# Kernel tuning notes

Measured on AMD Instinct MI355X. Metric: run time of the kernel, lower is better.

Reference implementation:

```python
import jax, jax.numpy as jnp
import numpy as np

N_NODES = 50000
N_EDGES = 800000
EPS = 1e-5


def setup_inputs() -> dict:
    key = jax.random.key(0)
    ks = jax.random.split(key, 8)
    x = jax.random.normal(ks[0], (N_NODES, 4), dtype=jnp.float32)
    edge_index = jax.random.randint(ks[1], (2, N_EDGES), 0, N_NODES, dtype=jnp.int64)
    edge_attr = jax.random.normal(ks[2], (N_EDGES, 84), dtype=jnp.float32)
    # nnconv1 (acts as Linear(88,128) over concatenated per-edge features)
    W1 = jax.random.normal(ks[3], (88, 128), dtype=jnp.float32) * (1.0 / np.sqrt(88))
    b1 = jnp.zeros((128,), dtype=jnp.float32)
    # BatchNorm1d(128) affine params
    gamma = jnp.ones((128,), dtype=jnp.float32)
    beta = jnp.zeros((128,), dtype=jnp.float32)
    # node_mlp_2: Linear(132,64) + ReLU
    W2 = jax.random.normal(ks[4], (132, 64), dtype=jnp.float32) * (1.0 / np.sqrt(132))
    b2 = jnp.zeros((64,), dtype=jnp.float32)
    return {"x": x, "edge_index": edge_index, "edge_attr": edge_attr,
            "W1": W1, "b1": b1, "gamma": gamma, "beta": beta, "W2": W2, "b2": b2}


def reference(x, edge_index, edge_attr, W1, b1, gamma, beta, W2, b2):
    row, col = edge_index[0], edge_index[1]
    n_nodes = x.shape[0]
    # gather + concat: [E, 4+84=88]
    h = jnp.concatenate([x[col], edge_attr], axis=1)
    # edge-conditioned linear (NNConv wrapper == Linear(88,128)): [E,128]
    h = h @ W1 + b1
    # BatchNorm1d over edge batch dim (training mode, biased var as torch)
    mean = jnp.mean(h, axis=0)
    var = jnp.mean((h - mean) ** 2, axis=0)
    h = (h - mean) * jax.lax.rsqrt(var + EPS) * gamma + beta
    # scatter_mean over row -> [N,128]
    agg = jax.ops.segment_sum(h, row, num_segments=n_nodes)
    cnt = jax.ops.segment_sum(jnp.ones((h.shape[0],), dtype=h.dtype), row,
                              num_segments=n_nodes)
    agg = agg / jnp.clip(cnt, 1.0)[:, None]
    # concat + MLP: [N, 4+128=132] -> [N,64]
    out = jnp.concatenate([x, agg], axis=1)
    return jax.nn.relu(out @ W2 + b2)
```

## Files before the change

### kernel.cpp

```cpp
#include <hip/hip_runtime.h>
#include <hip/hip_bf16.h>

#define E_EDGES 800000
#define N_NODES_ 50000
#define EPS_ 1e-5f
#define N_SCAN_BLOCKS 49

#define M_GRID   1250
#define M_ITERS  5
#define M_SPLITS 25

#define AGG_EPW  16

typedef float f32x4 __attribute__((ext_vector_type(4)));
typedef short s16x8 __attribute__((ext_vector_type(8)));

#define OFF_M      0
#define OFF_CS     (88 * 88)
#define OFF_CNT    (OFF_CS + 88)
#define OFF_AGG    (OFF_CNT + N_NODES_)
#define ZERO_WORDS (OFF_AGG + N_NODES_ * 88)
#define OFF_CUR    ZERO_WORDS
#define OFF_PART   (OFF_CUR + N_NODES_)
#define OFF_PERM   (OFF_PART + 64)
#define OFF_V      (OFF_PERM + E_EDGES)
#define OFF_S      (OFF_V + 88 * 128)
#define OFF_T      (OFF_S + 128)
#define OFF_MPART  (OFF_T + 128)

__global__ __launch_bounds__(256, 6)
void m_kernel(const float* __restrict__ x, const int* __restrict__ eidx,
              const float* __restrict__ ea, float* __restrict__ mpart)
{
    __shared__ __align__(16) short Gs_t[96 * 136];

    const int tid  = threadIdx.x;
    const int lane = tid & 63;
    const int wave = tid >> 6;
    const int m    = lane & 15;
    const int q    = lane >> 4;

    f32x4 acc[6];
#pragma unroll
    for (int i = 0; i < 6; ++i) acc[i] = (f32x4){0.f, 0.f, 0.f, 0.f};

    {
        int* gz = (int*)&Gs_t[88 * 136];
        for (int i = tid; i < 8 * 136 / 2; i += 256) gz[i] = 0;
    }

    unsigned addrL[21];
#pragma unroll
    for (int i = 0; i < 21; ++i) {
        const int d = (i * 256 + tid) * 2;
        const int e = d / 84;
        const int f = d - e * 84;
        addrL[i] = (unsigned)((4 + f) * 136 + e);
    }

    int tile = blockIdx.x;
    int colA = 0, colB = 0;
    if (tid < 128) colA = eidx[E_EDGES + tile * 128 + tid];
    float2 r[21];
    {
        const float2* tb = (const float2*)ea + (size_t)tile * 5376;
#pragma unroll
        for (int i = 0; i < 21; ++i) r[i] = tb[i * 256 + tid];
    }
    float4 xv = (float4){0.f, 0.f, 0.f, 0.f};
    if (tid < 128) xv = *(const float4*)(x + (size_t)colA * 4);
    if (tid < 128) colB = eidx[E_EDGES + (tile + M_GRID) * 128 + tid];

#pragma unroll 1
    for (int it = 0; it < M_ITERS; ++it) {
        __syncthreads();

        if (tid < 128) {
            __hip_bfloat16 b0 = __float2bfloat16(xv.x);
            __hip_bfloat16 b1 = __float2bfloat16(xv.y);
            __hip_bfloat16 b2 = __float2bfloat16(xv.z);
            __hip_bfloat16 b3 = __float2bfloat16(xv.w);
            Gs_t[0 * 136 + tid] = *(short*)&b0;
            Gs_t[1 * 136 + tid] = *(short*)&b1;
            Gs_t[2 * 136 + tid] = *(short*)&b2;
            Gs_t[3 * 136 + tid] = *(short*)&b3;
        }
#pragma unroll
        for (int i = 0; i < 21; ++i) {
            __hip_bfloat16 b0 = __float2bfloat16(r[i].x);
            __hip_bfloat16 b1 = __float2bfloat16(r[i].y);
            Gs_t[addrL[i]]       = *(short*)&b0;
            Gs_t[addrL[i] + 136] = *(short*)&b1;
        }

        const int next = tile + M_GRID;
        if (it + 1 < M_ITERS) {
            const float2* tbn = (const float2*)ea + (size_t)next * 5376;
#pragma unroll
            for (int i = 0; i < 21; ++i) r[i] = tbn[i * 256 + tid];
            if (tid < 128) xv = *(const float4*)(x + (size_t)colB * 4);
            if (tid < 128 && it + 2 < M_ITERS)
                colB = eidx[E_EDGES + (next + M_GRID) * 128 + tid];
        }
        __syncthreads();

#pragma unroll
        for (int kk = 0; kk < 4; ++kk) {
            const int kbase = kk * 32 + q * 8;
            s16x8 fr[6];
#pragma unroll
            for (int p = 0; p < 6; ++p)
                fr[p] = *reinterpret_cast<const s16x8*>(
                            &Gs_t[(p * 16 + m) * 136 + kbase]);
#define MM(i, a, b) acc[i] = __builtin_amdgcn_mfma_f32_16x16x32_bf16(fr[a], fr[b], acc[i], 0, 0, 0)
            if      (wave == 0) { MM(0,0,0); MM(1,0,4); MM(2,1,3); MM(3,2,3); MM(4,3,4); MM(5,5,5); }
            else if (wave == 1) { MM(0,0,1); MM(1,0,5); MM(2,1,4); MM(3,2,4); MM(4,3,5); }
            else if (wave == 2) { MM(0,0,2); MM(1,1,1); MM(2,1,5); MM(3,2,5); MM(4,4,4); }
            else                { MM(0,0,3); MM(1,1,2); MM(2,2,2); MM(3,3,3); MM(4,4,5); }
#undef MM
        }
        tile = next;
    }

    {
        float* pb = mpart + (size_t)blockIdx.x * 5376;
        const int nt = (wave == 0) ? 6 : 5;
#pragma unroll
        for (int i = 0; i < 6; ++i) {
            if (i < nt) {
                const int k = wave + i * 4;
                *(f32x4*)(pb + k * 256 + m * 16 + q * 4) = acc[i];
            }
        }
    }
}

__global__ __launch_bounds__(256)
void m_reduce_kernel(const float* __restrict__ mpart, float* __restrict__ M)
{
    const int g     = blockIdx.x * 256 + threadIdx.x;
    const int pos   = g % 5376;
    const int split = g / 5376;
    const int b0    = split * (M_GRID / M_SPLITS);
    const int b1    = b0 + (M_GRID / M_SPLITS);

    float s = 0.f;
#pragma unroll 5
    for (int b = b0; b < b1; ++b) s += mpart[(size_t)b * 5376 + pos];

    const int k  = pos >> 8;
    const int wi = pos & 255;
    const int m  = wi >> 4;
    const int qr = wi & 15;
    const int tr = (k >= 20) ? 5 : (k >= 18) ? 4 : (k >= 15) ? 3
                 : (k >= 11) ? 2 : (k >= 6) ? 1 : 0;
    const int S  = (tr == 5) ? 20 : (tr == 4) ? 18 : (tr == 3) ? 15
                 : (tr == 2) ? 11 : (tr == 1) ? 6 : 0;
    const int tc = tr + (k - S);
    const int rr = tr * 16 + qr;
    const int c  = tc * 16 + m;
    if (rr < 88 && c < 88) {
        atomicAdd(&M[rr * 88 + c], s);
        if (tr != tc) atomicAdd(&M[c * 88 + rr], s);
    }
}

__global__ void hist_kernel(const int* __restrict__ eidx, int* __restrict__ cnt)
{
    int e = blockIdx.x * 256 + threadIdx.x;
    if (e < E_EDGES) atomicAdd(&cnt[eidx[e]], 1);
}

__global__ void scan1_kernel(const int* __restrict__ cnt, int* __restrict__ partial)
{
    __shared__ int l[1024];
    int i = blockIdx.x * 1024 + threadIdx.x;
    l[threadIdx.x] = (i < N_NODES_) ? cnt[i] : 0;
    __syncthreads();
    for (int s = 512; s > 0; s >>= 1) {
        if (threadIdx.x < s) l[threadIdx.x] += l[threadIdx.x + s];
        __syncthreads();
    }
    if (threadIdx.x == 0) partial[blockIdx.x] = l[0];
}

__global__ void scan2_kernel(int* __restrict__ partial)
{
    if (threadIdx.x == 0) {
        int acc = 0;
        for (int i = 0; i < N_SCAN_BLOCKS; ++i) {
            int t = partial[i]; partial[i] = acc; acc += t;
        }
    }
}

__global__ void scan3_kernel(const int* __restrict__ cnt, const int* __restrict__ partial,
                             int* __restrict__ cursor)
{
    __shared__ int l[1024];
    int i = blockIdx.x * 1024 + threadIdx.x;
    int v = (i < N_NODES_) ? cnt[i] : 0;
    l[threadIdx.x] = v;
    __syncthreads();
    for (int s = 1; s < 1024; s <<= 1) {
        int t = (threadIdx.x >= s) ? l[threadIdx.x - s] : 0;
        __syncthreads();
        l[threadIdx.x] += t;
        __syncthreads();
    }
    if (i < N_NODES_) cursor[i] = partial[blockIdx.x] + l[threadIdx.x] - v;
}

__global__ void scatter_kernel(const int* __restrict__ eidx, int* __restrict__ cursor,
                               int* __restrict__ perm)
{
    int e = blockIdx.x * 256 + threadIdx.x;
    if (e < E_EDGES) {
        int pos = atomicAdd(&cursor[eidx[e]], 1);
        perm[pos] = e;
    }
}

__global__ __launch_bounds__(256)
void agg_kernel(const float* __restrict__ x, const int* __restrict__ eidx,
                const float* __restrict__ ea, const int* __restrict__ perm,
                float* __restrict__ agg)
{
    __shared__ int eL[4][AGG_EPW];
    __shared__ int rL[4][AGG_EPW];
    __shared__ int cL[4][AGG_EPW];

    const int tid  = threadIdx.x;
    const int lane = tid & 63;
    const int wv   = tid >> 6;
    const int base = (blockIdx.x * 4 + wv) * AGG_EPW;

    if (lane < AGG_EPW) {
        int e = perm[base + lane];
        eL[wv][lane] = e;
        rL[wv][lane] = eidx[e];
        cL[wv][lane] = eidx[E_EDGES + e];
    }
    __syncthreads();

    float a0 = 0.f, a1 = 0.f;
    int cur = rL[wv][0];
#pragma unroll
    for (int j = 0; j < AGG_EPW; ++j) {
        const int e   = eL[wv][j];
        const int row = rL[wv][j];
        const int col = cL[wv][j];
        const float* p = ea + (size_t)e * 84;
        float v0 = (lane < 4) ? x[(size_t)col * 4 + lane] : p[lane - 4];
        float v1 = (lane < 24) ? p[60 + lane] : 0.f;
        if (row != cur) {
            atomicAdd(&agg[(size_t)cur * 88 + lane], a0);
            if (lane < 24) atomicAdd(&agg[(size_t)cur * 88 + 64 + lane], a1);
            a0 = 0.f; a1 = 0.f; cur = row;
        }
        a0 += v0;
        a1 += v1;
    }
    atomicAdd(&agg[(size_t)cur * 88 + lane], a0);
    if (lane < 24) atomicAdd(&agg[(size_t)cur * 88 + 64 + lane], a1);
}

__global__ void colsum_kernel(const float* __restrict__ agg, float* __restrict__ cs)
{
    const int f = threadIdx.x;
    if (f >= 88) return;
    float a = 0.f;
    for (int n = blockIdx.x; n < N_NODES_; n += gridDim.x) a += agg[n * 88 + f];
    atomicAdd(&cs[f], a);
}

__global__ void mv_kernel(const float* __restrict__ M, const float* __restrict__ W1,
                          float* __restrict__ v)
{
    const int a = blockIdx.x;
    const int j = threadIdx.x;
    float acc = 0.f;
    for (int b = 0; b < 88; ++b) acc += M[a * 88 + b] * W1[b * 128 + j];
    v[a * 128 + j] = acc;
}

__global__ void stats_kernel(const float* __restrict__ cs, const float* __restrict__ v,
                             const float* __restrict__ W1, const float* __restrict__ b1,
                             const float* __restrict__ gamma, const float* __restrict__ beta,
                             float* __restrict__ s, float* __restrict__ t)
{
    const int j = threadIdx.x;
    const float invE = 1.0f / (float)E_EDGES;
    float mu = 0.f, eh2 = 0.f;
    for (int a = 0; a < 88; ++a) {
        float w = W1[a * 128 + j];
        mu  += cs[a] * w;
        eh2 += v[a * 128 + j] * w;
    }
    mu *= invE;
    eh2 *= invE;
    float var  = eh2 - mu * mu;
    float mean = mu + b1[j];
    float inv  = rsqrtf(var + EPS_);
    float sj   = gamma[j] * inv;
    s[j] = sj;
    t[j] = beta[j] - mean * sj;
}

__global__ __launch_bounds__(128)
void node_kernel(const float* __restrict__ x, const float* __restrict__ agg,
                 const int* __restrict__ cnt, const float* __restrict__ W1,
                 const float* __restrict__ b1, const float* __restrict__ W2,
                 const float* __restrict__ b2, const float* __restrict__ s,
                 const float* __restrict__ t, float* __restrict__ out)
{
    __shared__ float aggL[4 * 88];
    __shared__ float featL[4][128];
    __shared__ float cntL[4];
    __shared__ float xL[16];
    const int tid = threadIdx.x;
    const int nbase = blockIdx.x * 4;

    for (int i = tid; i < 352; i += 128) aggL[i] = agg[nbase * 88 + i];
    if (tid < 4)  cntL[tid] = (float)cnt[nbase + tid];
    if (tid < 16) xL[tid] = x[nbase * 4 + tid];
    __syncthreads();

    {
        const int j = tid;
        float a0 = 0.f, a1 = 0.f, a2 = 0.f, a3 = 0.f;
        for (int a = 0; a < 88; ++a) {
            float w = W1[a * 128 + j];
            a0 += aggL[a]       * w;
            a1 += aggL[88 + a]  * w;
            a2 += aggL[176 + a] * w;
            a3 += aggL[264 + a] * w;
        }
        const float sj = s[j], tj = t[j], bj = b1[j];
        float accs[4] = {a0, a1, a2, a3};
#pragma unroll
        for (int n = 0; n < 4; ++n) {
            float c = cntL[n];
            featL[n][j] = (c > 0.f) ? (sj * (accs[n] / c + bj) + tj) : 0.f;
        }
    }
    __syncthreads();

    {
        const int jc = tid & 63;
        const int nh = tid >> 6;
#pragma unroll
        for (int h = 0; h < 2; ++h) {
            const int n = nh * 2 + h;
            float acc = b2[jc];
#pragma unroll
            for (int k = 0; k < 4; ++k) acc += xL[n * 4 + k] * W2[k * 64 + jc];
            for (int k = 0; k < 128; ++k)
                acc += featL[n][k] * W2[(4 + k) * 64 + jc];
            out[(nbase + n) * 64 + jc] = fmaxf(acc, 0.f);
        }
    }
}

extern "C" void kernel_launch(void* const* d_in, const int* in_sizes, int n_in,
                              void* d_out, int out_size, void* d_ws, size_t ws_size,
                              hipStream_t stream)
{
    const float* x     = (const float*)d_in[0];
    const int*   eidx  = (const int*)d_in[1];
    const float* ea    = (const float*)d_in[2];
    const float* W1    = (const float*)d_in[3];
    const float* b1    = (const float*)d_in[4];
    const float* gamma = (const float*)d_in[5];
    const float* beta  = (const float*)d_in[6];
    const float* W2    = (const float*)d_in[7];
    const float* b2    = (const float*)d_in[8];

    float* ws    = (float*)d_ws;
    float* M     = ws + OFF_M;
    float* cs    = ws + OFF_CS;
    int*   cnt   = (int*)(ws + OFF_CNT);
    float* agg   = ws + OFF_AGG;
    int*   cur   = (int*)(ws + OFF_CUR);
    int*   part  = (int*)(ws + OFF_PART);
    int*   perm  = (int*)(ws + OFF_PERM);
    float* v     = ws + OFF_V;
    float* s     = ws + OFF_S;
    float* t     = ws + OFF_T;
    float* mpart = ws + OFF_MPART;
    float* out   = (float*)d_out;

    hipMemsetAsync(d_ws, 0, (size_t)ZERO_WORDS * sizeof(float), stream);

    hist_kernel<<<(E_EDGES + 255) / 256, 256, 0, stream>>>(eidx, cnt);
    scan1_kernel<<<N_SCAN_BLOCKS, 1024, 0, stream>>>(cnt, part);
    scan2_kernel<<<1, 64, 0, stream>>>(part);
    scan3_kernel<<<N_SCAN_BLOCKS, 1024, 0, stream>>>(cnt, part, cur);
    scatter_kernel<<<(E_EDGES + 255) / 256, 256, 0, stream>>>(eidx, cur, perm);

    m_kernel<<<M_GRID, 256, 0, stream>>>(x, eidx, ea, mpart);
    m_reduce_kernel<<<(5376 * M_SPLITS) / 256, 256, 0, stream>>>(mpart, M);
    agg_kernel<<<E_EDGES / (4 * AGG_EPW), 256, 0, stream>>>(x, eidx, ea, perm, agg);

    colsum_kernel<<<512, 96, 0, stream>>>(agg, cs);
    mv_kernel<<<88, 128, 0, stream>>>(M, W1, v);
    stats_kernel<<<1, 128, 0, stream>>>(cs, v, W1, b1, gamma, beta, s, t);
    node_kernel<<<12500, 128, 0, stream>>>(x, agg, cnt, W1, b1, W2, b2, s, t, out);
}
```

Measured before the change: 837.6 us.

## Fuse Gram-matrix MFMA pass with sorted edge aggregation in one kernel

Replaces the separate m_kernel and agg_kernel with one fused kernel. It walks edges in row-sorted perm order and loads each edge's x[col] and edge_attr row once. That data feeds two consumers: the bf16 LDS tile used for the 88x88 Gram-matrix MFMA, and an fp32 LDS copy with XOR swizzling that a per-feature serial loop segment-sums into agg with atomics. The aim is to remove the second full read of edge_attr. In exchange it uses gathered row loads instead of contiguous tiles, doubles LDS use (2 blocks/CU), halves the grid, and adds a serial 128-step aggregation loop on only 22 lanes per wave inside each tile iteration.

```diff
diff --git a/kernel.cpp b/kernel.cpp
--- a/kernel.cpp
+++ b/kernel.cpp
@@ -6,11 +6,9 @@
 #define EPS_ 1e-5f
 #define N_SCAN_BLOCKS 49
 
-#define M_GRID   1250
-#define M_ITERS  5
+#define M_GRID   625
+#define M_TILES  10
 #define M_SPLITS 25
-
-#define AGG_EPW  16
 
 typedef float f32x4 __attribute__((ext_vector_type(4)));
 typedef short s16x8 __attribute__((ext_vector_type(8)));
@@ -28,17 +26,22 @@
 #define OFF_T      (OFF_S + 128)
 #define OFF_MPART  (OFF_T + 128)
 
-__global__ __launch_bounds__(256, 6)
-void m_kernel(const float* __restrict__ x, const int* __restrict__ eidx,
-              const float* __restrict__ ea, float* __restrict__ mpart)
+__global__ __launch_bounds__(256, 2)
+void fused_kernel(const float* __restrict__ x, const int* __restrict__ eidx,
+                  const float* __restrict__ ea, const int* __restrict__ perm,
+                  float* __restrict__ mpart, float* __restrict__ agg)
 {
     __shared__ __align__(16) short Gs_t[96 * 136];
+    __shared__ __align__(16) float EAf[128 * 96];
+    __shared__ int rL[128];
 
     const int tid  = threadIdx.x;
     const int lane = tid & 63;
     const int wave = tid >> 6;
     const int m    = lane & 15;
     const int q    = lane >> 4;
+    const int slot = tid & 127;
+    const int h    = tid >> 7;
 
     f32x4 acc[6];
 #pragma unroll
@@ -49,58 +52,83 @@
         for (int i = tid; i < 8 * 136 / 2; i += 256) gz[i] = 0;
     }
 
-    unsigned addrL[21];
-#pragma unroll
-    for (int i = 0; i < 21; ++i) {
-        const int d = (i * 256 + tid) * 2;
-        const int e = d / 84;
-        const int f = d - e * 84;
-        addrL[i] = (unsigned)((4 + f) * 136 + e);
-    }
-
     int tile = blockIdx.x;
-    int colA = 0, colB = 0;
-    if (tid < 128) colA = eidx[E_EDGES + tile * 128 + tid];
-    float2 r[21];
+    int pe   = perm[tile * 128 + slot];
+    int rowe = eidx[pe];
+    int cole = eidx[E_EDGES + pe];
+    f32x4 rf[12];
     {
-        const float2* tb = (const float2*)ea + (size_t)tile * 5376;
-#pragma unroll
-        for (int i = 0; i < 21; ++i) r[i] = tb[i * 256 + tid];
-    }
-    float4 xv = (float4){0.f, 0.f, 0.f, 0.f};
-    if (tid < 128) xv = *(const float4*)(x + (size_t)colA * 4);
-    if (tid < 128) colB = eidx[E_EDGES + (tile + M_GRID) * 128 + tid];
+        const float* er = ea + (size_t)pe * 84;
+        if (h == 0) {
+#pragma unroll
+            for (int i = 0; i < 11; ++i) rf[i + 1] = *(const f32x4*)(er + i * 4);
+            rf[0] = *(const f32x4*)(x + (size_t)cole * 4);
+        } else {
+#pragma unroll
+            for (int i = 0; i < 10; ++i) rf[i] = *(const f32x4*)(er + 44 + i * 4);
+        }
+    }
+    int pf = perm[(tile + M_GRID) * 128 + slot];
 
 #pragma unroll 1
-    for (int it = 0; it < M_ITERS; ++it) {
+    for (int it = 0; it < M_TILES; ++it) {
         __syncthreads();
 
-        if (tid < 128) {
-            __hip_bfloat16 b0 = __float2bfloat16(xv.x);
-            __hip_bfloat16 b1 = __float2bfloat16(xv.y);
-            __hip_bfloat16 b2 = __float2bfloat16(xv.z);
-            __hip_bfloat16 b3 = __float2bfloat16(xv.w);
-            Gs_t[0 * 136 + tid] = *(short*)&b0;
-            Gs_t[1 * 136 + tid] = *(short*)&b1;
-            Gs_t[2 * 136 + tid] = *(short*)&b2;
-            Gs_t[3 * 136 + tid] = *(short*)&b3;
-        }
-#pragma unroll
-        for (int i = 0; i < 21; ++i) {
-            __hip_bfloat16 b0 = __float2bfloat16(r[i].x);
-            __hip_bfloat16 b1 = __float2bfloat16(r[i].y);
-            Gs_t[addrL[i]]       = *(short*)&b0;
-            Gs_t[addrL[i] + 136] = *(short*)&b1;
-        }
-
-        const int next = tile + M_GRID;
-        if (it + 1 < M_ITERS) {
-            const float2* tbn = (const float2*)ea + (size_t)next * 5376;
-#pragma unroll
-            for (int i = 0; i < 21; ++i) r[i] = tbn[i * 256 + tid];
-            if (tid < 128) xv = *(const float4*)(x + (size_t)colB * 4);
-            if (tid < 128 && it + 2 < M_ITERS)
-                colB = eidx[E_EDGES + (next + M_GRID) * 128 + tid];
+        if (h == 0) {
+#pragma unroll
+            for (int j = 0; j < 4; ++j) {
+                __hip_bfloat16 b = __float2bfloat16(rf[0][j]);
+                Gs_t[j * 136 + slot] = *(short*)&b;
+            }
+#pragma unroll
+            for (int i = 0; i < 11; ++i) {
+#pragma unroll
+                for (int j = 0; j < 4; ++j) {
+                    __hip_bfloat16 b = __float2bfloat16(rf[i + 1][j]);
+                    Gs_t[(4 + i * 4 + j) * 136 + slot] = *(short*)&b;
+                }
+            }
+            rL[slot] = rowe;
+        } else {
+#pragma unroll
+            for (int i = 0; i < 10; ++i) {
+#pragma unroll
+                for (int j = 0; j < 4; ++j) {
+                    __hip_bfloat16 b = __float2bfloat16(rf[i][j]);
+                    Gs_t[(48 + i * 4 + j) * 136 + slot] = *(short*)&b;
+                }
+            }
+        }
+        {
+            const int k  = (slot & 7) << 2;
+            float* base  = EAf + slot * 96;
+            if (h == 0) {
+                *(f32x4*)(base + (0 ^ k)) = rf[0];
+#pragma unroll
+                for (int i = 0; i < 11; ++i)
+                    *(f32x4*)(base + ((4 + 4 * i) ^ k)) = rf[i + 1];
+            } else {
+#pragma unroll
+                for (int i = 0; i < 10; ++i)
+                    *(f32x4*)(base + ((48 + 4 * i) ^ k)) = rf[i];
+            }
+        }
+
+        if (it + 1 < M_TILES) {
+            pe   = pf;
+            rowe = eidx[pe];
+            cole = eidx[E_EDGES + pe];
+            const float* er = ea + (size_t)pe * 84;
+            if (h == 0) {
+#pragma unroll
+                for (int i = 0; i < 11; ++i) rf[i + 1] = *(const f32x4*)(er + i * 4);
+                rf[0] = *(const f32x4*)(x + (size_t)cole * 4);
+            } else {
+#pragma unroll
+                for (int i = 0; i < 10; ++i) rf[i] = *(const f32x4*)(er + 44 + i * 4);
+            }
+            if (it + 2 < M_TILES)
+                pf = perm[(tile + (it + 2) * M_GRID) * 128 + slot];
         }
         __syncthreads();
 
@@ -119,7 +147,23 @@
             else                { MM(0,0,3); MM(1,1,2); MM(2,2,2); MM(3,3,3); MM(4,4,5); }
 #undef MM
         }
-        tile = next;
+
+        if (lane < 22) {
+            const int f = wave * 22 + lane;
+            float a  = 0.f;
+            int  cur = rL[0];
+#pragma unroll 8
+            for (int s = 0; s < 128; ++s) {
+                const int   row = rL[s];
+                const float v   = EAf[s * 96 + (f ^ ((s & 7) << 2))];
+                if (row != cur) {
+                    atomicAdd(&agg[(size_t)cur * 88 + f], a);
+                    a = 0.f; cur = row;
+                }
+                a += v;
+            }
+            atomicAdd(&agg[(size_t)cur * 88 + f], a);
+        }
     }
 
     {
@@ -221,50 +265,6 @@
     }
 }
 
-__global__ __launch_bounds__(256)
-void agg_kernel(const float* __restrict__ x, const int* __restrict__ eidx,
-                const float* __restrict__ ea, const int* __restrict__ perm,
-                float* __restrict__ agg)
-{
-    __shared__ int eL[4][AGG_EPW];
-    __shared__ int rL[4][AGG_EPW];
-    __shared__ int cL[4][AGG_EPW];
-
-    const int tid  = threadIdx.x;
-    const int lane = tid & 63;
-    const int wv   = tid >> 6;
-    const int base = (blockIdx.x * 4 + wv) * AGG_EPW;
-
-    if (lane < AGG_EPW) {
-        int e = perm[base + lane];
-        eL[wv][lane] = e;
-        rL[wv][lane] = eidx[e];
-        cL[wv][lane] = eidx[E_EDGES + e];
-    }
-    __syncthreads();
-
-    float a0 = 0.f, a1 = 0.f;
-    int cur = rL[wv][0];
-#pragma unroll
-    for (int j = 0; j < AGG_EPW; ++j) {
-        const int e   = eL[wv][j];
-        const int row = rL[wv][j];
-        const int col = cL[wv][j];
-        const float* p = ea + (size_t)e * 84;
-        float v0 = (lane < 4) ? x[(size_t)col * 4 + lane] : p[lane - 4];
-        float v1 = (lane < 24) ? p[60 + lane] : 0.f;
-        if (row != cur) {
-            atomicAdd(&agg[(size_t)cur * 88 + lane], a0);
-            if (lane < 24) atomicAdd(&agg[(size_t)cur * 88 + 64 + lane], a1);
-            a0 = 0.f; a1 = 0.f; cur = row;
-        }
-        a0 += v0;
-        a1 += v1;
-    }
-    atomicAdd(&agg[(size_t)cur * 88 + lane], a0);
-    if (lane < 24) atomicAdd(&agg[(size_t)cur * 88 + 64 + lane], a1);
-}
-
 __global__ void colsum_kernel(const float* __restrict__ agg, float* __restrict__ cs)
 {
     const int f = threadIdx.x;
@@ -398,9 +398,8 @@
     scan3_kernel<<<N_SCAN_BLOCKS, 1024, 0, stream>>>(cnt, part, cur);
     scatter_kernel<<<(E_EDGES + 255) / 256, 256, 0, stream>>>(eidx, cur, perm);
 
-    m_kernel<<<M_GRID, 256, 0, stream>>>(x, eidx, ea, mpart);
+    fused_kernel<<<M_GRID, 256, 0, stream>>>(x, eidx, ea, perm, mpart, agg);
     m_reduce_kernel<<<(5376 * M_SPLITS) / 256, 256, 0, stream>>>(mpart, M);
-    agg_kernel<<<E_EDGES / (4 * AGG_EPW), 256, 0, stream>>>(x, eidx, ea, perm, agg);
 
     colsum_kernel<<<512, 96, 0, stream>>>(agg, cs);
     mv_kernel<<<88, 128, 0, stream>>>(M, W1, v);
```

Result: faster. 784.4 us (-6.3%).
